# Kernel tuning notes

Measured on AMD Instinct MI355X. Metric: run time of the kernel, lower is better.

The kernel has to match this reference:

```python
import jax, jax.numpy as jnp
import numpy as np

E = 256          # embedding_dim
H = 2 * E        # lstm hidden = 512
L = 2 * E        # seq_len must equal 2*E for the attn_weights * x broadcast
B = 32
NH = 8           # attention heads
HD = H // NH     # head dim = 64


def _lstm_layer(x, Wih, Whh, bih, bhh):
    # x: [B, L, Din] -> [B, L, H]. PyTorch gate order: i, f, g, o.
    b = x.shape[0]
    h0 = jnp.zeros((b, H), x.dtype)
    c0 = jnp.zeros((b, H), x.dtype)

    def step(carry, xt):
        h, c = carry
        gates = xt @ Wih.T + h @ Whh.T + (bih + bhh)  # [B, 4H]
        i, f, g, o = jnp.split(gates, 4, axis=-1)
        i = jax.nn.sigmoid(i)
        f = jax.nn.sigmoid(f)
        g = jnp.tanh(g)
        o = jax.nn.sigmoid(o)
        c = f * c + i * g
        h = o * jnp.tanh(c)
        return (h, c), h

    _, hs = jax.lax.scan(step, (h0, c0), x.transpose(1, 0, 2))  # hs: [L, B, H]
    return hs.transpose(1, 0, 2)


def setup_inputs() -> dict:
    key = jax.random.key(0)
    ks = jax.random.split(key, 16)
    s = 0.02
    inp = {
        "x": jax.random.normal(ks[0], (B, L, E), jnp.float32),
        # LSTM layer 0 (input E -> hidden H)
        "Wih0": jax.random.normal(ks[1], (4 * H, E), jnp.float32) * s,
        "Whh0": jax.random.normal(ks[2], (4 * H, H), jnp.float32) * s,
        "bih0": jnp.zeros((4 * H,), jnp.float32),
        "bhh0": jnp.zeros((4 * H,), jnp.float32),
        # LSTM layer 1 (H -> H)
        "Wih1": jax.random.normal(ks[3], (4 * H, H), jnp.float32) * s,
        "Whh1": jax.random.normal(ks[4], (4 * H, H), jnp.float32) * s,
        "bih1": jnp.zeros((4 * H,), jnp.float32),
        "bhh1": jnp.zeros((4 * H,), jnp.float32),
        # MHA q/k projections (v and out_proj are dead: only attn weights used)
        "Wq": jax.random.normal(ks[5], (H, H), jnp.float32) * s,
        "bq": jnp.zeros((H,), jnp.float32),
        "Wk": jax.random.normal(ks[6], (H, H), jnp.float32) * s,
        "bk": jnp.zeros((H,), jnp.float32),
        # output linear H -> 1
        "Wo": jax.random.normal(ks[7], (1, H), jnp.float32) * s,
        "bo": jnp.zeros((1,), jnp.float32),
    }
    return inp


def reference(x, Wih0, Whh0, bih0, bhh0, Wih1, Whh1, bih1, bhh1,
              Wq, bq, Wk, bk, Wo, bo):
    # 2-layer LSTM
    h = _lstm_layer(x, Wih0, Whh0, bih0, bhh0)   # [B, L, H]
    h = _lstm_layer(h, Wih1, Whh1, bih1, bhh1)   # [B, L, H]

    # MHA attention weights (averaged over heads), causal mask, scale 1/sqrt(HD)
    q = (h @ Wq.T + bq).reshape(B, L, NH, HD)
    k = (h @ Wk.T + bk).reshape(B, L, NH, HD)
    scores = jnp.einsum("bqhd,bkhd->bhqk", q, k) / jnp.sqrt(jnp.float32(HD))
    causal = jnp.tril(jnp.ones((L, L), bool))
    scores = jnp.where(causal[None, None], scores, -jnp.inf)
    attn = jax.nn.softmax(scores, axis=-1)       # [B, NH, L, L]
    attn_w = attn.mean(axis=1)                   # [B, L, L], avg over heads

    # elementwise gate (valid because L == H) and final linear
    gated = attn_w * h                            # [B, L, H]
    return gated @ Wo.T + bo                      # [B, L, 1]
```

## Files before the change

kernel.cpp:

```cpp
#include <hip/hip_runtime.h>
#include <cmath>

#define NBAT 32
#define PADH2 6
#define NWG  256

__device__ __forceinline__ float sigf(float x) { return 1.f / (1.f + __expf(-x)); }

__device__ __forceinline__ float2 f2fma(float2 a, float s, float2 c) {
  return make_float2(fmaf(a.x, s, c.x), fmaf(a.y, s, c.y));
}

__device__ __forceinline__ int gswz(int c) { return c ^ (c >> 3); }

__global__ __launch_bounds__(256, 2) void gemm128(
    const float* __restrict__ A, const float* __restrict__ B,
    const float* __restrict__ bias1, const float* __restrict__ bias2,
    float* __restrict__ C, int M, int N, int K, int gmode) {
  __shared__ __align__(16) float As[8][132];
  __shared__ __align__(16) float Bs[8][132];
  const int tid = threadIdx.x;
  const int n0 = blockIdx.x * 128, m0 = blockIdx.y * 128;
  const int lm = tid & 127, kh = tid >> 7;
  const int tx = tid & 15, ty = tid >> 4;
  const int colp = (gswz(lm >> 2) << 2) | (lm & 3);
  const int ca0 = gswz(2 * ty) * 4, ca1 = gswz(2 * ty + 1) * 4;
  const int cb0 = gswz(2 * tx) * 4, cb1 = gswz(2 * tx + 1) * 4;
  const float* Ap = A + (size_t)(m0 + lm) * K + kh * 4;
  const float* Bp = B + (size_t)(n0 + lm) * K + kh * 4;
  float acc[8][8] = {};
  float4 av = *(const float4*)Ap;
  float4 bv = *(const float4*)Bp;
  const int nk = K / 8;
  for (int kt = 0; kt < nk; ++kt) {
    __syncthreads();
    As[kh*4+0][colp] = av.x; As[kh*4+1][colp] = av.y;
    As[kh*4+2][colp] = av.z; As[kh*4+3][colp] = av.w;
    Bs[kh*4+0][colp] = bv.x; Bs[kh*4+1][colp] = bv.y;
    Bs[kh*4+2][colp] = bv.z; Bs[kh*4+3][colp] = bv.w;
    __syncthreads();
    if (kt + 1 < nk) {
      av = *(const float4*)(Ap + (kt + 1) * 8);
      bv = *(const float4*)(Bp + (kt + 1) * 8);
    }
#pragma unroll
    for (int kk = 0; kk < 8; ++kk) {
      float4 a0 = *(const float4*)&As[kk][ca0];
      float4 a1 = *(const float4*)&As[kk][ca1];
      float4 b0 = *(const float4*)&Bs[kk][cb0];
      float4 b1 = *(const float4*)&Bs[kk][cb1];
      float ar[8] = {a0.x,a0.y,a0.z,a0.w,a1.x,a1.y,a1.z,a1.w};
      float br[8] = {b0.x,b0.y,b0.z,b0.w,b1.x,b1.y,b1.z,b1.w};
#pragma unroll
      for (int i = 0; i < 8; ++i)
#pragma unroll
        for (int j = 0; j < 8; ++j)
          acc[i][j] += ar[i] * br[j];
    }
  }
  const int nc = n0 + tx * 8;
  float bb[8];
  { float4 c0 = *(const float4*)&bias1[nc], c1 = *(const float4*)&bias1[nc+4];
    bb[0]=c0.x; bb[1]=c0.y; bb[2]=c0.z; bb[3]=c0.w;
    bb[4]=c1.x; bb[5]=c1.y; bb[6]=c1.z; bb[7]=c1.w; }
  if (bias2) {
    float4 c0 = *(const float4*)&bias2[nc], c1 = *(const float4*)&bias2[nc+4];
    bb[0]+=c0.x; bb[1]+=c0.y; bb[2]+=c0.z; bb[3]+=c0.w;
    bb[4]+=c1.x; bb[5]+=c1.y; bb[6]+=c1.z; bb[7]+=c1.w;
  }
#pragma unroll
  for (int i = 0; i < 8; ++i) {
    const int m = m0 + ty * 8 + i;
    float4 o0 = make_float4(acc[i][0]+bb[0], acc[i][1]+bb[1], acc[i][2]+bb[2], acc[i][3]+bb[3]);
    float4 o1 = make_float4(acc[i][4]+bb[4], acc[i][5]+bb[5], acc[i][6]+bb[6], acc[i][7]+bb[7]);
    if (gmode) {
      const int b = m >> 9, tt = m & 511, g = nc >> 9, j = nc & 511;
      const size_t base = ((size_t)(tt * 4 + g) * 32 + b) * 512 + j;
      *(float4*)&C[base] = o0; *(float4*)&C[base + 4] = o1;
    } else {
      *(float4*)&C[(size_t)m * N + nc] = o0;
      *(float4*)&C[(size_t)m * N + nc + 4] = o1;
    }
  }
}

__global__ __launch_bounds__(256, 1) void lstm_rec(
    const float* __restrict__ G,
    const float* __restrict__ Whh,
    float* __restrict__ Hout,
    float2* __restrict__ hT2) {
  __shared__ __align__(16) float h_lds[512 * PADH2];
  __shared__ __align__(16) float red2[4][16][20];
  __shared__ __align__(16) float pre_s[2][4][4][16];

  const int tid = threadIdx.x;
  const int wg  = blockIdx.x;
  const int bg  = wg >> 5;
  const int jg  = wg & 31;
  const int j0  = jg * 16;
  const int lane = tid & 63;
  const int wv   = tid >> 6;

  const int kq = tid >> 4;
  const int jj = tid & 15;

  float w_reg[32][4];
#pragma unroll
  for (int g = 0; g < 4; ++g) {
    const float* wrow = Whh + (size_t)(g * 512 + j0 + jj) * 512 + kq;
#pragma unroll
    for (int i = 0; i < 32; ++i) w_reg[i][g] = wrow[16 * i];
  }

  const int ob  = tid >> 4;
  const int ojj = tid & 15;
  float c_reg = 0.f;

  const int pid = tid - 128;
  const int pg = pid >> 5, pb = (pid >> 3) & 3, pjh = pid & 7;
  float2 gpre;
  if (tid >= 128)
    gpre = *(const float2*)&G[(((size_t)0 * 4 + pg) * 32 + bg * 4 + pb) * 512 + j0 + pjh * 2];

  const size_t dom = (size_t)bg * 2048;

  for (int t = 0; t < 512; ++t) {
    const int buf = t & 1;

    if (tid >= 128)
      *(float2*)&pre_s[buf][pg][pb][pjh * 2] = gpre;

    const float* h2f = (const float*)(hT2 + (size_t)buf * 16384 + dom);
    const float ftag = (float)t;
    float4 hv[4];
#pragma unroll
    for (int it = 0; it < 4; ++it)
      asm volatile("global_load_dwordx4 %0, %1, off sc0 sc1"
                   : "=&v"(hv[it])
                   : "v"(h2f + (size_t)(tid + it * 256) * 4));
    asm volatile("s_waitcnt vmcnt(0)" ::: "memory");
    for (;;) {
      bool ok = true;
#pragma unroll
      for (int it = 0; it < 4; ++it)
        ok = ok && (hv[it].y == ftag) && (hv[it].w == ftag);
      if (__all(ok)) break;
#pragma unroll
      for (int it = 0; it < 4; ++it)
        if (hv[it].y != ftag || hv[it].w != ftag)
          asm volatile("global_load_dwordx4 %0, %1, off sc0 sc1"
                       : "=&v"(hv[it])
                       : "v"(h2f + (size_t)(tid + it * 256) * 4));
      asm volatile("s_waitcnt vmcnt(0)" ::: "memory");
    }
    __builtin_amdgcn_sched_barrier(0);
#pragma unroll
    for (int it = 0; it < 4; ++it) {
      const int idx4 = tid + it * 256;
      *(float2*)&h_lds[(idx4 >> 1) * PADH2 + (idx4 & 1) * 2] =
          make_float2(hv[it].x, hv[it].z);
    }
    __syncthreads();

    if (tid >= 128 && t + 1 < 512)
      gpre = *(const float2*)&G[(((size_t)(t + 1) * 4 + pg) * 32 + bg * 4 + pb) * 512 + j0 + pjh * 2];

    float2 acc2[2][4] = {};
#pragma unroll
    for (int i = 0; i < 32; ++i) {
      const int k = kq + 16 * i;
      const float2* hp2 = (const float2*)&h_lds[k * PADH2];
      float2 h01 = hp2[0], h23 = hp2[1];
#pragma unroll
      for (int g = 0; g < 4; ++g) {
        const float w = w_reg[i][g];
        acc2[0][g] = f2fma(h01, w, acc2[0][g]);
        acc2[1][g] = f2fma(h23, w, acc2[1][g]);
      }
    }
    float acc[4][4];
#pragma unroll
    for (int x = 0; x < 2; ++x)
#pragma unroll
      for (int g = 0; g < 4; ++g) {
        acc[2*x][g]   = acc2[x][g].x;
        acc[2*x+1][g] = acc2[x][g].y;
      }

#pragma unroll
    for (int bl = 0; bl < 4; ++bl)
#pragma unroll
      for (int g = 0; g < 4; ++g) {
        float v = acc[bl][g];
        v += __shfl_down(v, 32, 64);
        v += __shfl_down(v, 16, 64);
        acc[bl][g] = v;
      }
    if (lane < 16) {
#pragma unroll
      for (int e = 0; e < 16; ++e) red2[wv][lane][e] = acc[e >> 2][e & 3];
    }
    __syncthreads();

    if (tid < 64) {
      float4 s0 = *(const float4*)&red2[0][ojj][ob * 4];
      float4 s1 = *(const float4*)&red2[1][ojj][ob * 4];
      float4 s2 = *(const float4*)&red2[2][ojj][ob * 4];
      float4 s3 = *(const float4*)&red2[3][ojj][ob * 4];
      const float gi = (s0.x + s1.x) + (s2.x + s3.x) + pre_s[buf][0][ob][ojj];
      const float gf = (s0.y + s1.y) + (s2.y + s3.y) + pre_s[buf][1][ob][ojj];
      const float gg = (s0.z + s1.z) + (s2.z + s3.z) + pre_s[buf][2][ob][ojj];
      const float go = (s0.w + s1.w) + (s2.w + s3.w) + pre_s[buf][3][ob][ojj];
      const float iv = sigf(gi);
      const float fv = sigf(gf);
      const float gv = tanhf(gg);
      const float ov = sigf(go);
      const float c = fv * c_reg + iv * gv;
      c_reg = c;
      const float h = ov * tanhf(c);
      float2* hnxt = hT2 + (size_t)((t + 1) & 1) * 16384 + dom;
      const float2 pub = make_float2(h, (float)(t + 1));
      asm volatile("global_store_dwordx2 %0, %1, off sc0 sc1"
                   :: "v"(&hnxt[(j0 + ojj) * 4 + ob]), "v"(pub) : "memory");
      Hout[((size_t)(bg * 4 + ob) * 512 + t) * 512 + j0 + ojj] = h;
    }
  }
}

__device__ __forceinline__ int kswz(int row, int col) {
  return row * 64 + (col ^ (((row >> 2) & 7) << 2));
}

__global__ __launch_bounds__(256) void attn_kernel(
    const float* __restrict__ Qg, const float* __restrict__ Kg,
    const float* __restrict__ H2, const float* __restrict__ Wo,
    const float* __restrict__ bo, float* __restrict__ out) {
  __shared__ float Ks[64 * 64];
  __shared__ float part[4][16][68];
  __shared__ float s[16][512];
  __shared__ float Wo_s[512];

  const int tid = threadIdx.x;
  const int qt = blockIdx.x, b = blockIdx.y;
  const int q0 = qt * 16;
  const int dd = tid >> 6, qq = (tid >> 4) & 3, kq = tid & 15;
  const int srow = tid >> 4, slane = tid & 15;

  Wo_s[tid] = Wo[tid];
  Wo_s[256 + tid] = Wo[256 + tid];

  float out_reg = 0.f;
  const int kcmax = (q0 + 15) >> 6;

  for (int h = 0; h < 8; ++h) {
    float qreg[4][16];
#pragma unroll
    for (int r = 0; r < 4; ++r) {
      const float* qrow = Qg + ((size_t)(b * 512) + q0 + qq * 4 + r) * 512 + h * 64 + dd * 16;
#pragma unroll
      for (int i = 0; i < 16; i += 4) {
        float4 v = *(const float4*)(qrow + i);
        qreg[r][i] = v.x; qreg[r][i+1] = v.y; qreg[r][i+2] = v.z; qreg[r][i+3] = v.w;
      }
    }

    for (int kc = 0; kc <= kcmax; ++kc) {
      __syncthreads();
#pragma unroll
      for (int it = 0; it < 4; ++it) {
        const int f = tid * 4 + it * 1024;
        const int kk = f >> 6, d = f & 63;
        float4 v = *(const float4*)(Kg + ((size_t)(b * 512) + kc * 64 + kk) * 512 + h * 64 + d);
        Ks[kswz(d + 0, kk)] = v.x;
        Ks[kswz(d + 1, kk)] = v.y;
        Ks[kswz(d + 2, kk)] = v.z;
        Ks[kswz(d + 3, kk)] = v.w;
      }
      __syncthreads();

      float acc[4][4] = {};
#pragma unroll
      for (int i = 0; i < 16; ++i) {
        const int row = dd * 16 + i;
        float4 k4 = *(const float4*)&Ks[kswz(row, kq * 4)];
#pragma unroll
        for (int r = 0; r < 4; ++r) {
          acc[r][0] += qreg[r][i] * k4.x;
          acc[r][1] += qreg[r][i] * k4.y;
          acc[r][2] += qreg[r][i] * k4.z;
          acc[r][3] += qreg[r][i] * k4.w;
        }
      }
#pragma unroll
      for (int r = 0; r < 4; ++r)
        *(float4*)&part[dd][qq * 4 + r][kq * 4] =
            make_float4(acc[r][0], acc[r][1], acc[r][2], acc[r][3]);
      __syncthreads();
      {
        const int qi = tid >> 4, c = tid & 15;
        float4 p0 = *(const float4*)&part[0][qi][c * 4];
        float4 p1 = *(const float4*)&part[1][qi][c * 4];
        float4 p2 = *(const float4*)&part[2][qi][c * 4];
        float4 p3 = *(const float4*)&part[3][qi][c * 4];
        float4 r;
        r.x = ((p0.x + p1.x) + (p2.x + p3.x)) * 0.125f;
        r.y = ((p0.y + p1.y) + (p2.y + p3.y)) * 0.125f;
        r.z = ((p0.z + p1.z) + (p2.z + p3.z)) * 0.125f;
        r.w = ((p0.w + p1.w) + (p2.w + p3.w)) * 0.125f;
        *(float4*)&s[qi][kc * 64 + c * 4] = r;
      }
    }
    __syncthreads();

    const int q = q0 + srow;
    const int count = q + 1;
    const float* sp = &s[srow][0];
    float m = -1e30f;
    for (int d = slane; d < count; d += 16) m = fmaxf(m, sp[d]);
    m = fmaxf(m, __shfl_xor(m, 1, 64));
    m = fmaxf(m, __shfl_xor(m, 2, 64));
    m = fmaxf(m, __shfl_xor(m, 4, 64));
    m = fmaxf(m, __shfl_xor(m, 8, 64));
    float z = 0.f, zw = 0.f;
    const float* h2row = H2 + ((size_t)(b * 512) + q) * 512;
    for (int d = slane; d < count; d += 16) {
      const float e = __expf(sp[d] - m);
      z += e;
      zw += e * h2row[d] * Wo_s[d];
    }
    z += __shfl_xor(z, 1, 64); z += __shfl_xor(z, 2, 64);
    z += __shfl_xor(z, 4, 64); z += __shfl_xor(z, 8, 64);
    zw += __shfl_xor(zw, 1, 64); zw += __shfl_xor(zw, 2, 64);
    zw += __shfl_xor(zw, 4, 64); zw += __shfl_xor(zw, 8, 64);
    out_reg += zw / z;
    __syncthreads();
  }

  if (slane == 0)
    out[b * 512 + q0 + srow] = out_reg * 0.125f + bo[0];
}

extern "C" void kernel_launch(void* const* d_in, const int* in_sizes, int n_in,
                              void* d_out, int out_size, void* d_ws, size_t ws_size,
                              hipStream_t stream) {
  const float* x    = (const float*)d_in[0];
  const float* Wih0 = (const float*)d_in[1];
  const float* Whh0 = (const float*)d_in[2];
  const float* bih0 = (const float*)d_in[3];
  const float* bhh0 = (const float*)d_in[4];
  const float* Wih1 = (const float*)d_in[5];
  const float* Whh1 = (const float*)d_in[6];
  const float* bih1 = (const float*)d_in[7];
  const float* bhh1 = (const float*)d_in[8];
  const float* Wq   = (const float*)d_in[9];
  const float* bq   = (const float*)d_in[10];
  const float* Wk   = (const float*)d_in[11];
  const float* bk   = (const float*)d_in[12];
  const float* Wo   = (const float*)d_in[13];
  const float* bo   = (const float*)d_in[14];
  float* out = (float*)d_out;

  float* ws = (float*)d_ws;
  const size_t M = 16384;
  float* G  = ws;
  float* H1 = G  + (size_t)16384 * 2048;
  float* H2 = H1 + (size_t)16384 * 512;
  float2* hT2 = (float2*)(H2 + (size_t)16384 * 512);
  float* Qb = H1;
  float* Kb = G;

  hipMemsetAsync(hT2, 0, 2 * 16384 * sizeof(float2), stream);

  gemm128<<<dim3(2048 / 128, M / 128), 256, 0, stream>>>(x, Wih0, bih0, bhh0, G,
                                                         (int)M, 2048, 256, 1);
  lstm_rec<<<NWG, 256, 0, stream>>>(G, Whh0, H1, hT2);

  hipMemsetAsync(hT2, 0, 2 * 16384 * sizeof(float2), stream);
  gemm128<<<dim3(2048 / 128, M / 128), 256, 0, stream>>>(H1, Wih1, bih1, bhh1, G,
                                                         (int)M, 2048, 512, 1);
  lstm_rec<<<NWG, 256, 0, stream>>>(G, Whh1, H2, hT2);

  gemm128<<<dim3(512 / 128, M / 128), 256, 0, stream>>>(H2, Wq, bq, nullptr, Qb,
                                                        (int)M, 512, 512, 0);
  gemm128<<<dim3(512 / 128, M / 128), 256, 0, stream>>>(H2, Wk, bk, nullptr, Kb,
                                                        (int)M, 512, 512, 0);

  attn_kernel<<<dim3(32, 32), 256, 0, stream>>>(Qb, Kb, H2, Wo, bo, out);
}
```

Before: 4.846 ms.

## Replace tagged h-value polling with per-batch-group atomic counter barrier in LSTM recurrence

The recurrent kernel used to publish each hidden value together with a step tag and spin on the data until every tag matched. It now publishes plain floats, waits for the wave's stores to complete, and bumps a per-batch-group atomic counter. Consumers spin on that counter, with a short sleep between polls, before loading the hidden state. This halves the exchanged data and the polling traffic. In exchange it adds a store-wait, an atomic, and a second dependent global round trip on every timestep's critical path.

```diff
diff --git a/kernel.cpp b/kernel.cpp
--- a/kernel.cpp
+++ b/kernel.cpp
@@ -2,7 +2,7 @@
 #include <cmath>
 
 #define NBAT 32
-#define PADH2 6
+#define HROW 6
 #define NWG  256
 
 __device__ __forceinline__ float sigf(float x) { return 1.f / (1.f + __expf(-x)); }
@@ -88,8 +88,10 @@
     const float* __restrict__ G,
     const float* __restrict__ Whh,
     float* __restrict__ Hout,
-    float2* __restrict__ hT2) {
-  __shared__ __align__(16) float h_lds[512 * PADH2];
+    float* __restrict__ hT,
+    int* __restrict__ cnt,
+    int gen_base) {
+  __shared__ __align__(16) float h_lds[512 * HROW];
   __shared__ __align__(16) float red2[4][16][20];
   __shared__ __align__(16) float pre_s[2][4][4][16];
 
@@ -123,6 +125,7 @@
     gpre = *(const float2*)&G[(((size_t)0 * 4 + pg) * 32 + bg * 4 + pb) * 512 + j0 + pjh * 2];
 
   const size_t dom = (size_t)bg * 2048;
+  int* cp = cnt + bg;
 
   for (int t = 0; t < 512; ++t) {
     const int buf = t & 1;
@@ -130,35 +133,31 @@
     if (tid >= 128)
       *(float2*)&pre_s[buf][pg][pb][pjh * 2] = gpre;
 
-    const float* h2f = (const float*)(hT2 + (size_t)buf * 16384 + dom);
-    const float ftag = (float)t;
-    float4 hv[4];
-#pragma unroll
-    for (int it = 0; it < 4; ++it)
+    {
+      const int target = (gen_base + t) * 32;
+      for (;;) {
+        int c0;
+        asm volatile("global_load_dword %0, %1, off sc0 sc1\n\ts_waitcnt vmcnt(0)"
+                     : "=&v"(c0) : "v"(cp) : "memory");
+        if (c0 >= target) break;
+        __builtin_amdgcn_s_sleep(2);
+      }
+    }
+
+    const float* h2f = hT + (size_t)buf * 16384 + dom;
+    float4 hv[2];
+#pragma unroll
+    for (int it = 0; it < 2; ++it)
       asm volatile("global_load_dwordx4 %0, %1, off sc0 sc1"
                    : "=&v"(hv[it])
                    : "v"(h2f + (size_t)(tid + it * 256) * 4));
     asm volatile("s_waitcnt vmcnt(0)" ::: "memory");
-    for (;;) {
-      bool ok = true;
-#pragma unroll
-      for (int it = 0; it < 4; ++it)
-        ok = ok && (hv[it].y == ftag) && (hv[it].w == ftag);
-      if (__all(ok)) break;
-#pragma unroll
-      for (int it = 0; it < 4; ++it)
-        if (hv[it].y != ftag || hv[it].w != ftag)
-          asm volatile("global_load_dwordx4 %0, %1, off sc0 sc1"
-                       : "=&v"(hv[it])
-                       : "v"(h2f + (size_t)(tid + it * 256) * 4));
-      asm volatile("s_waitcnt vmcnt(0)" ::: "memory");
-    }
     __builtin_amdgcn_sched_barrier(0);
 #pragma unroll
-    for (int it = 0; it < 4; ++it) {
-      const int idx4 = tid + it * 256;
-      *(float2*)&h_lds[(idx4 >> 1) * PADH2 + (idx4 & 1) * 2] =
-          make_float2(hv[it].x, hv[it].z);
+    for (int it = 0; it < 2; ++it) {
+      const int j = tid + it * 256;
+      *(float2*)&h_lds[j * HROW]     = make_float2(hv[it].x, hv[it].y);
+      *(float2*)&h_lds[j * HROW + 2] = make_float2(hv[it].z, hv[it].w);
     }
     __syncthreads();
 
@@ -169,7 +168,7 @@
 #pragma unroll
     for (int i = 0; i < 32; ++i) {
       const int k = kq + 16 * i;
-      const float2* hp2 = (const float2*)&h_lds[k * PADH2];
+      const float2* hp2 = (const float2*)&h_lds[k * HROW];
       float2 h01 = hp2[0], h23 = hp2[1];
 #pragma unroll
       for (int g = 0; g < 4; ++g) {
@@ -218,10 +217,15 @@
       const float c = fv * c_reg + iv * gv;
       c_reg = c;
       const float h = ov * tanhf(c);
-      float2* hnxt = hT2 + (size_t)((t + 1) & 1) * 16384 + dom;
-      const float2 pub = make_float2(h, (float)(t + 1));
-      asm volatile("global_store_dwordx2 %0, %1, off sc0 sc1"
-                   :: "v"(&hnxt[(j0 + ojj) * 4 + ob]), "v"(pub) : "memory");
+      float* hnxt = hT + (size_t)((t + 1) & 1) * 16384 + dom;
+      asm volatile("global_store_dword %0, %1, off sc0 sc1"
+                   :: "v"(&hnxt[(j0 + ojj) * 4 + ob]), "v"(h) : "memory");
+      asm volatile("s_waitcnt vmcnt(0)" ::: "memory");
+      if (tid == 0) {
+        const int one = 1;
+        asm volatile("global_atomic_add %0, %1, off sc1"
+                     :: "v"(cp), "v"(one) : "memory");
+      }
       Hout[((size_t)(bg * 4 + ob) * 512 + t) * 512 + j0 + ojj] = h;
     }
   }
@@ -365,20 +369,21 @@
   float* G  = ws;
   float* H1 = G  + (size_t)16384 * 2048;
   float* H2 = H1 + (size_t)16384 * 512;
-  float2* hT2 = (float2*)(H2 + (size_t)16384 * 512);
+  float* hT = H2 + (size_t)16384 * 512;
+  int* cnt  = (int*)(hT + 2 * 16384);
   float* Qb = H1;
   float* Kb = G;
 
-  hipMemsetAsync(hT2, 0, 2 * 16384 * sizeof(float2), stream);
+  hipMemsetAsync(hT, 0, 2 * 16384 * sizeof(float) + 8 * sizeof(int), stream);
 
   gemm128<<<dim3(2048 / 128, M / 128), 256, 0, stream>>>(x, Wih0, bih0, bhh0, G,
                                                          (int)M, 2048, 256, 1);
-  lstm_rec<<<NWG, 256, 0, stream>>>(G, Whh0, H1, hT2);
-
-  hipMemsetAsync(hT2, 0, 2 * 16384 * sizeof(float2), stream);
+  lstm_rec<<<NWG, 256, 0, stream>>>(G, Whh0, H1, hT, cnt, 0);
+
+  hipMemsetAsync(hT, 0, 2 * 16384 * sizeof(float), stream);
   gemm128<<<dim3(2048 / 128, M / 128), 256, 0, stream>>>(H1, Wih1, bih1, bhh1, G,
                                                          (int)M, 2048, 512, 1);
-  lstm_rec<<<NWG, 256, 0, stream>>>(G, Whh1, H2, hT2);
+  lstm_rec<<<NWG, 256, 0, stream>>>(G, Whh1, H2, hT, cnt, 512);
 
   gemm128<<<dim3(512 / 128, M / 128), 256, 0, stream>>>(H2, Wq, bq, nullptr, Qb,
                                                         (int)M, 512, 512, 0);
```

Result: slower. 18.68 ms, median of 3 (+285.5%).
